# Kernel optimization log

Hardware: AMD Instinct MI355X
Metric: run time of the kernel (lower is better)

The kernel has to match this reference:

```python
import jax, jax.numpy as jnp
import numpy as np

N_ENT = 50000     # n_entities
C = 128           # channel
N_EDGES = 1600000 # n_edges (avg degree 32)
N_REL = 11        # n_relations; edge_type in [1, N_REL-1]
N_HOPS = 3
EPS = 1e-12       # F.normalize default eps


def setup_inputs() -> dict:
    key = jax.random.key(0)
    k1, k2, k3, k4 = jax.random.split(key, 4)
    entity_emb = jax.random.normal(k1, (N_ENT, C), dtype=jnp.float32)
    edge_index = jax.random.randint(k2, (2, N_EDGES), 0, N_ENT, dtype=jnp.int64)
    edge_type = jax.random.randint(k3, (N_EDGES,), 1, N_REL, dtype=jnp.int64)
    # xavier_uniform bound for (N_REL-1, C)
    bound = float(np.sqrt(6.0 / ((N_REL - 1) + C)))
    weight = jax.random.uniform(k4, (N_REL - 1, C), jnp.float32, -bound, bound)
    return {"entity_emb": entity_emb, "edge_index": edge_index,
            "edge_type": edge_type, "weight": weight}


def reference(entity_emb, edge_index, edge_type, weight):
    head, tail = edge_index[0], edge_index[1]
    # relation embedding per edge: weight[edge_type - 1] -> [E, C]
    rel_emb = weight[edge_type - 1]
    ones = jnp.ones((edge_index.shape[1],), entity_emb.dtype)
    # per-head in-degree counts (constant across hops)
    cnt = jax.ops.segment_sum(ones, head, num_segments=N_ENT)
    denom = jnp.maximum(cnt, 1.0)[:, None]  # scatter_mean: zero rows stay zero

    def hop(emb):
        msg = emb[tail] * rel_emb                                   # gather + mul [E, C]
        agg = jax.ops.segment_sum(msg, head, num_segments=N_ENT) / denom  # scatter_mean
        # F.normalize (L2 per row)
        norm = jnp.linalg.norm(agg, axis=1, keepdims=True)
        return agg / jnp.maximum(norm, EPS)

    res = entity_emb
    emb = entity_emb
    for _ in range(N_HOPS):
        emb = hop(emb)
        res = res + emb
    return res
```

## Files before the change

kernel.cpp:

```cpp
#include <hip/hip_runtime.h>

#define N_ENT   50000
#define CH      128
#define N_EDGES 1600000
#define N_RELM1 10
#define NB      391
#define BCAP    4608
#define PART_BLOCKS 800
#define CHUNK   (N_EDGES / PART_BLOCKS)
#define EPS_N   1e-12f

__device__ __forceinline__ unsigned int f2bf_bits(float f) {
    unsigned int x = __float_as_uint(f);
    return (x + 0x7FFFu + ((x >> 16) & 1u)) >> 16;
}

__global__ __launch_bounds__(256) void gc_part_kernel(const int* __restrict__ head,
                                                      const int* __restrict__ tail,
                                                      const int* __restrict__ etyp,
                                                      int* __restrict__ barr,
                                                      int* __restrict__ pack,
                                                      const float* __restrict__ ent,
                                                      unsigned int* __restrict__ emb) {
    __shared__ int hist[512];
    __shared__ int boff_s[512];
    __shared__ int fctr[512];
    __shared__ int psum[256];
    __shared__ int stageE[CHUNK];
    __shared__ unsigned short stageB[CHUNK];
    __shared__ int stage2[CHUNK];
    int tid = threadIdx.x, blk = blockIdx.x;
    for (int i = tid; i < 512; i += 256) { hist[i] = 0; fctr[i] = 0; }
    __syncthreads();
    int lo = blk * CHUNK;
    for (int i = tid; i < CHUNK; i += 256) {
        int e = lo + i;
        int h = head[e];
        int b = h >> 7;
        stageE[i] = (tail[e] & 0xFFFF) | ((etyp[e] - 1) << 16) | ((h & 127) << 20);
        stageB[i] = (unsigned short)b;
        atomicAdd(&hist[b], 1);
    }
    __syncthreads();
    int a0 = hist[2 * tid], a1 = hist[2 * tid + 1];
    int s2 = a0 + a1;
    psum[tid] = s2;
    __syncthreads();
    for (int d = 1; d < 256; d <<= 1) {
        int t = (tid >= d) ? psum[tid - d] : 0;
        __syncthreads();
        psum[tid] += t;
        __syncthreads();
    }
    int excl = psum[tid] - s2;
    boff_s[2 * tid] = excl;
    boff_s[2 * tid + 1] = excl + a0;
    __syncthreads();
    for (int i = tid; i < CHUNK; i += 256) {
        int b = stageB[i];
        int pos = boff_s[b] + atomicAdd(&fctr[b], 1);
        stage2[pos] = stageE[i];
    }
    __syncthreads();
    for (int i = tid; i < CHUNK; i += 256) barr[lo + i] = stage2[i];
    for (int i = tid; i < NB; i += 256)
        pack[blk * NB + i] = (boff_s[i] << 8) | fctr[i];
    for (int i = blk * 256 + tid; i < N_ENT * (CH / 2); i += PART_BLOCKS * 256) {
        float2 v = *(const float2*)(ent + 2 * (size_t)i);
        emb[i] = f2bf_bits(v.x) | (f2bf_bits(v.y) << 16);
    }
}

__global__ __launch_bounds__(1024) void gc_place_kernel(const int* __restrict__ barr,
                                                        const int* __restrict__ pack,
                                                        unsigned int* __restrict__ off_deg,
                                                        int* __restrict__ csr) {
    __shared__ int ent_s[BCAP];
    __shared__ int psum[1024];
    __shared__ int hcnt[128];
    __shared__ int hloc[128];
    __shared__ int hctr[128];
    int b = blockIdx.x, tid = threadIdx.x;
    if (tid < 128) { hcnt[tid] = 0; hctr[tid] = 0; }
    int c = 0, o = 0;
    if (tid < PART_BLOCKS) {
        int pk = pack[tid * NB + b];
        c = pk & 255;
        o = pk >> 8;
    }
    psum[tid] = c;
    __syncthreads();
    for (int d = 1; d < 1024; d <<= 1) {
        int t = (tid >= d) ? psum[tid - d] : 0;
        __syncthreads();
        psum[tid] += t;
        __syncthreads();
    }
    int my_off = psum[tid] - c;
    int n = psum[1023];
    const int* src = barr + tid * CHUNK + o;
    for (int k = 0; k < c; ++k) ent_s[my_off + k] = src[k];
    __syncthreads();
    for (int i = tid; i < n; i += 1024)
        atomicAdd(&hcnt[(ent_s[i] >> 20) & 127], 1);
    __syncthreads();
    int v = (tid < 128) ? hcnt[tid] : 0;
    for (int d = 1; d < 128; d <<= 1) {
        int t = (tid < 128 && tid >= d) ? hcnt[tid - d] : 0;
        __syncthreads();
        if (tid < 128) hcnt[tid] += t;
        __syncthreads();
    }
    int lo = b * BCAP;
    if (tid < 128) {
        int start = lo + hcnt[tid] - v;
        hloc[tid] = start;
        int h = (b << 7) + tid;
        if (h < N_ENT) off_deg[h] = ((unsigned)start << 11) | (unsigned)v;
    }
    __syncthreads();
    for (int i = tid; i < n; i += 1024) {
        int e = ent_s[i];
        int hl = (e >> 20) & 127;
        int pos = hloc[hl] + atomicAdd(&hctr[hl], 1);
        csr[pos] = e & 0xFFFFF;
    }
}

__global__ __launch_bounds__(256) void gc_hop_kernel(
        const unsigned int* __restrict__ src,
        const unsigned int* __restrict__ off_deg,
        const int* __restrict__ csr,
        const float* __restrict__ wt,
        unsigned int* __restrict__ dst,
        float* __restrict__ res,
        const float* __restrict__ ent,
        int init) {
    __shared__ float wt_s[N_RELM1 * CH];
    for (int i = threadIdx.x; i < N_RELM1 * CH; i += 256) wt_s[i] = wt[i];
    __syncthreads();

    int wave = threadIdx.x >> 6, lane = threadIdx.x & 63;
    int row = __builtin_amdgcn_readfirstlane(blockIdx.x * 4 + wave);

    unsigned od = (unsigned)__builtin_amdgcn_readfirstlane((int)off_deg[row]);
    int seg = (int)(od >> 11);
    int deg = (int)(od & 2047u);
    int seg_end = seg + deg;

    float ax = 0.f, ay = 0.f;
    int j = seg;
    for (; j + 8 <= seg_end; j += 8) {
        int pk[8];
        #pragma unroll
        for (int u = 0; u < 8; ++u)
            pk[u] = __builtin_amdgcn_readfirstlane(csr[j + u]);
        #pragma unroll
        for (int u = 0; u < 8; ++u) {
            unsigned v = src[pk[u] % 65536 * 64 + lane];
            float2 w = *(const float2*)(&wt_s[(pk[u] >> 16) * CH + 2 * lane]);
            ax = fmaf(__uint_as_float(v << 16), w.x, ax);
            ay = fmaf(__uint_as_float(v & 0xFFFF0000u), w.y, ay);
        }
    }
    for (; j < seg_end; ++j) {
        int pk = __builtin_amdgcn_readfirstlane(csr[j]);
        unsigned v = src[pk % 65536 * 64 + lane];
        float2 w = *(const float2*)(&wt_s[(pk >> 16) * CH + 2 * lane]);
        ax = fmaf(__uint_as_float(v << 16), w.x, ax);
        ay = fmaf(__uint_as_float(v & 0xFFFF0000u), w.y, ay);
    }

    float invd = 1.0f / fmaxf((float)deg, 1.0f);
    float x0 = ax * invd, x1 = ay * invd;

    float s = x0 * x0 + x1 * x1;
    #pragma unroll
    for (int o = 32; o > 0; o >>= 1) s += __shfl_down(s, o, 64);
    s = __shfl(s, 0, 64);

    float inv = 1.0f / fmaxf(sqrtf(s), EPS_N);
    float y0 = x0 * inv, y1 = x1 * inv;

    dst[(row << 6) + lane] = f2bf_bits(y0) | (f2bf_bits(y1) << 16);

    int base = (row << 7) + 2 * lane;
    if (init) {
        float2 e = *(const float2*)(ent + base);
        *(float2*)(res + base) = make_float2(e.x + y0, e.y + y1);
    } else {
        float2 rv = *(const float2*)(res + base);
        *(float2*)(res + base) = make_float2(rv.x + y0, rv.y + y1);
    }
}

extern "C" void kernel_launch(void* const* d_in, const int* in_sizes, int n_in,
                              void* d_out, int out_size, void* d_ws, size_t ws_size,
                              hipStream_t stream) {
    const float* ent  = (const float*)d_in[0];
    const int*   eidx = (const int*)d_in[1];
    const int*   etyp = (const int*)d_in[2];
    const float* wt   = (const float*)d_in[3];
    float*       res  = (float*)d_out;

    const int* head = eidx;
    const int* tail = eidx + N_EDGES;

    unsigned int* embA = (unsigned int*)d_ws;
    unsigned int* embB = embA + (size_t)N_ENT * 64;
    int* barr  = (int*)(embB + (size_t)N_ENT * 64);
    int* pack  = barr + N_EDGES;
    unsigned int* off_deg = (unsigned int*)(pack + PART_BLOCKS * NB);
    int* csr   = (int*)(off_deg + N_ENT);

    gc_part_kernel<<<PART_BLOCKS, 256, 0, stream>>>(head, tail, etyp, barr, pack,
                                                    ent, embA);
    gc_place_kernel<<<NB, 1024, 0, stream>>>(barr, pack, off_deg, csr);

    const int hop_grid = N_ENT / 4;
    gc_hop_kernel<<<hop_grid, 256, 0, stream>>>(embA, off_deg, csr, wt, embB, res, ent, 1);
    gc_hop_kernel<<<hop_grid, 256, 0, stream>>>(embB, off_deg, csr, wt, embA, res, ent, 0);
    gc_hop_kernel<<<hop_grid, 256, 0, stream>>>(embA, off_deg, csr, wt, embB, res, ent, 0);
}
```

Baseline: 300.5 us.

## Prefetch CSR via scalar dwordx16 loads and fuse residual sum into final hop

The hop kernel now fetches CSR edge indices 16 at a time with inline-asm s_load_dwordx16, double-buffered so the next chunk loads while the current 16 edges are gathered. The residual accumulation is deferred to the last hop, which rebuilds ent + y1 + y2 + y3 from the bf16 intermediate buffers. This removes the fp32 res read/write traffic in the first two hops. The wave reduction switches to xor shuffles. The trade-off is that y1 and y2 enter the residual at bf16 precision, and the scalar loads may read past a row's segment end, which the reordered workspace layout has to absorb.

```diff
diff --git a/kernel.cpp b/kernel.cpp
--- a/kernel.cpp
+++ b/kernel.cpp
@@ -10,9 +10,21 @@
 #define CHUNK   (N_EDGES / PART_BLOCKS)
 #define EPS_N   1e-12f
 
+typedef int v16i __attribute__((ext_vector_type(16)));
+
 __device__ __forceinline__ unsigned int f2bf_bits(float f) {
     unsigned int x = __float_as_uint(f);
     return (x + 0x7FFFu + ((x >> 16) & 1u)) >> 16;
+}
+
+__device__ __forceinline__ v16i sload16(const int* p, int boff) {
+    v16i r;
+    asm volatile("s_load_dwordx16 %0, %1, %2"
+                 : "=s"(r) : "s"(p), "s"(boff));
+    return r;
+}
+__device__ __forceinline__ void swait16(v16i& r) {
+    asm volatile("s_waitcnt lgkmcnt(0)" : "+s"(r));
 }
 
 __global__ __launch_bounds__(256) void gc_part_kernel(const int* __restrict__ head,
@@ -135,7 +147,8 @@
         unsigned int* __restrict__ dst,
         float* __restrict__ res,
         const float* __restrict__ ent,
-        int init) {
+        const unsigned int* __restrict__ yprev,
+        int mode) {
     __shared__ float wt_s[N_RELM1 * CH];
     for (int i = threadIdx.x; i < N_RELM1 * CH; i += 256) wt_s[i] = wt[i];
     __syncthreads();
@@ -146,51 +159,57 @@
     unsigned od = (unsigned)__builtin_amdgcn_readfirstlane((int)off_deg[row]);
     int seg = (int)(od >> 11);
     int deg = (int)(od & 2047u);
-    int seg_end = seg + deg;
 
     float ax = 0.f, ay = 0.f;
-    int j = seg;
-    for (; j + 8 <= seg_end; j += 8) {
-        int pk[8];
+
+#define EDGE(pk) { \
+        unsigned v = src[(unsigned)((pk) & 0xFFFF) * 64u + (unsigned)lane]; \
+        float2 w = *(const float2*)(&wt_s[((pk) >> 16) * CH + 2 * lane]);   \
+        ax = fmaf(__uint_as_float(v << 16), w.x, ax);                       \
+        ay = fmaf(__uint_as_float(v & 0xFFFF0000u), w.y, ay); }
+
+    if (deg > 0) {
+        int nch = (deg + 15) >> 4;
+        v16i A = sload16(csr, seg << 2);
+        swait16(A);
+        int boff = (seg + 16) << 2;
+        for (int c = 0; c < nch - 1; ++c, boff += 64) {
+            v16i B = sload16(csr, boff);
+            #pragma unroll
+            for (int u = 0; u < 16; ++u) EDGE(A[u]);
+            swait16(B);
+            A = B;
+        }
+        int rem = deg - ((nch - 1) << 4);
         #pragma unroll
-        for (int u = 0; u < 8; ++u)
-            pk[u] = __builtin_amdgcn_readfirstlane(csr[j + u]);
-        #pragma unroll
-        for (int u = 0; u < 8; ++u) {
-            unsigned v = src[pk[u] % 65536 * 64 + lane];
-            float2 w = *(const float2*)(&wt_s[(pk[u] >> 16) * CH + 2 * lane]);
-            ax = fmaf(__uint_as_float(v << 16), w.x, ax);
-            ay = fmaf(__uint_as_float(v & 0xFFFF0000u), w.y, ay);
-        }
-    }
-    for (; j < seg_end; ++j) {
-        int pk = __builtin_amdgcn_readfirstlane(csr[j]);
-        unsigned v = src[pk % 65536 * 64 + lane];
-        float2 w = *(const float2*)(&wt_s[(pk >> 16) * CH + 2 * lane]);
-        ax = fmaf(__uint_as_float(v << 16), w.x, ax);
-        ay = fmaf(__uint_as_float(v & 0xFFFF0000u), w.y, ay);
-    }
+        for (int u = 0; u < 16; ++u)
+            if (u < rem) EDGE(A[u]);
+    }
+#undef EDGE
 
     float invd = 1.0f / fmaxf((float)deg, 1.0f);
     float x0 = ax * invd, x1 = ay * invd;
 
     float s = x0 * x0 + x1 * x1;
     #pragma unroll
-    for (int o = 32; o > 0; o >>= 1) s += __shfl_down(s, o, 64);
-    s = __shfl(s, 0, 64);
+    for (int o = 32; o; o >>= 1) s += __shfl_xor(s, o, 64);
 
     float inv = 1.0f / fmaxf(sqrtf(s), EPS_N);
-    float y0 = x0 * inv, y1 = x1 * inv;
-
-    dst[(row << 6) + lane] = f2bf_bits(y0) | (f2bf_bits(y1) << 16);
-
-    int base = (row << 7) + 2 * lane;
-    if (init) {
+    float y0 = x0 * inv, y1v = x1 * inv;
+
+    if (mode == 0) {
+        dst[(row << 6) + lane] = f2bf_bits(y0) | (f2bf_bits(y1v) << 16);
+    } else {
+        unsigned p1 = yprev[(row << 6) + lane];
+        unsigned p2 = src[(row << 6) + lane];
+        int base = (row << 7) + 2 * lane;
         float2 e = *(const float2*)(ent + base);
-        *(float2*)(res + base) = make_float2(e.x + y0, e.y + y1);
-    } else {
-        float2 rv = *(const float2*)(res + base);
-        *(float2*)(res + base) = make_float2(rv.x + y0, rv.y + y1);
+        float2 o;
+        o.x = e.x + __uint_as_float(p1 << 16)
+                  + __uint_as_float(p2 << 16) + y0;
+        o.y = e.y + __uint_as_float(p1 & 0xFFFF0000u)
+                  + __uint_as_float(p2 & 0xFFFF0000u) + y1v;
+        *(float2*)(res + base) = o;
     }
 }
 
@@ -208,17 +227,20 @@
 
     unsigned int* embA = (unsigned int*)d_ws;
     unsigned int* embB = embA + (size_t)N_ENT * 64;
-    int* barr  = (int*)(embB + (size_t)N_ENT * 64);
-    int* pack  = barr + N_EDGES;
-    unsigned int* off_deg = (unsigned int*)(pack + PART_BLOCKS * NB);
-    int* csr   = (int*)(off_deg + N_ENT);
+    unsigned int* off_deg = embB + (size_t)N_ENT * 64;
+    int* csr  = (int*)(off_deg + N_ENT);
+    int* barr = csr + (size_t)NB * BCAP;
+    int* pack = barr + N_EDGES;
 
     gc_part_kernel<<<PART_BLOCKS, 256, 0, stream>>>(head, tail, etyp, barr, pack,
                                                     ent, embA);
     gc_place_kernel<<<NB, 1024, 0, stream>>>(barr, pack, off_deg, csr);
 
     const int hop_grid = N_ENT / 4;
-    gc_hop_kernel<<<hop_grid, 256, 0, stream>>>(embA, off_deg, csr, wt, embB, res, ent, 1);
-    gc_hop_kernel<<<hop_grid, 256, 0, stream>>>(embB, off_deg, csr, wt, embA, res, ent, 0);
-    gc_hop_kernel<<<hop_grid, 256, 0, stream>>>(embA, off_deg, csr, wt, embB, res, ent, 0);
-}
+    gc_hop_kernel<<<hop_grid, 256, 0, stream>>>(embA, off_deg, csr, wt, embB,
+                                                res, ent, embB, 0);
+    gc_hop_kernel<<<hop_grid, 256, 0, stream>>>(embB, off_deg, csr, wt, embA,
+                                                res, ent, embB, 0);
+    gc_hop_kernel<<<hop_grid, 256, 0, stream>>>(embA, off_deg, csr, wt, embB,
+                                                res, ent, embB, 1);
+}
```

New measurement: 296.7 us. Within noise of the previous version (-1.2%).
